# Kernel tuning notes

Hardware: AMD Instinct MI355X
Metric: run time of the kernel (lower is better)

The kernel has to match this reference:

```python
import jax, jax.numpy as jnp
import numpy as np

B, S, HID = 1, 4096, 2048
H, KV, D = 16, 8, 128
EPS = 1e-6
ROPE_THETA = 10000.0


def _rms_norm(x, w, eps=EPS):
    # x: [..., D], normalize over last dim in fp32 like Qwen3 RMSNorm
    xf = x.astype(jnp.float32)
    var = jnp.mean(xf * xf, axis=-1, keepdims=True)
    return (xf * jax.lax.rsqrt(var + eps)).astype(x.dtype) * w


def _rotate_half(x):
    x1, x2 = jnp.split(x, 2, axis=-1)
    return jnp.concatenate([-x2, x1], axis=-1)


def setup_inputs() -> dict:
    key = jax.random.key(0)
    ks = jax.random.split(key, 6)
    hidden_states = jax.random.normal(ks[0], (B, S, HID), dtype=jnp.float32)
    wq = jax.random.normal(ks[1], (H * D, HID), dtype=jnp.float32) * 0.02
    wk = jax.random.normal(ks[2], (KV * D, HID), dtype=jnp.float32) * 0.02
    wv = jax.random.normal(ks[3], (KV * D, HID), dtype=jnp.float32) * 0.02
    wo = jax.random.normal(ks[4], (HID, H * D), dtype=jnp.float32) * 0.02
    q_norm_w = jnp.ones((D,), dtype=jnp.float32)
    k_norm_w = jnp.ones((D,), dtype=jnp.float32)
    # real rotary tables: inv_freq over half dim, duplicated (HF convention)
    inv_freq = 1.0 / (ROPE_THETA ** (jnp.arange(0, D, 2, dtype=jnp.float32) / D))
    pos = jnp.arange(S, dtype=jnp.float32)
    freqs = pos[:, None] * inv_freq[None, :]          # [S, D/2]
    emb = jnp.concatenate([freqs, freqs], axis=-1)    # [S, D]
    cos = jnp.cos(emb)[None].astype(jnp.float32)      # [B, S, D]
    sin = jnp.sin(emb)[None].astype(jnp.float32)
    return {"hidden_states": hidden_states, "cos": cos, "sin": sin,
            "wq": wq, "wk": wk, "wv": wv, "wo": wo,
            "q_norm_w": q_norm_w, "k_norm_w": k_norm_w}


def reference(hidden_states, cos, sin, wq, wk, wv, wo, q_norm_w, k_norm_w):
    b, s, _ = hidden_states.shape
    scaling = D ** -0.5
    # QKV projections (no bias), reshape to heads, QK RMSNorm, then [b, h, s, d]
    q = _rms_norm(jnp.einsum('bsh,oh->bso', hidden_states, wq).reshape(b, s, H, D), q_norm_w)
    k = _rms_norm(jnp.einsum('bsh,oh->bso', hidden_states, wk).reshape(b, s, KV, D), k_norm_w)
    v = jnp.einsum('bsh,oh->bso', hidden_states, wv).reshape(b, s, KV, D)
    q = q.transpose(0, 2, 1, 3)  # [b, H, s, d]
    k = k.transpose(0, 2, 1, 3)  # [b, KV, s, d]
    v = v.transpose(0, 2, 1, 3)
    # RoPE (cos/sin broadcast over head dim)
    c = cos[:, None, :, :]
    sn = sin[:, None, :, :]
    q = q * c + _rotate_half(q) * sn
    k = k * c + _rotate_half(k) * sn
    # GQA: repeat KV heads to H
    groups = H // KV
    k = jnp.repeat(k, groups, axis=1)
    v = jnp.repeat(v, groups, axis=1)
    # eager causal attention, softmax in fp32
    scores = jnp.einsum('bhqd,bhkd->bhqk', q, k) * scaling
    causal = jnp.tril(jnp.ones((s, s), dtype=bool))
    scores = jnp.where(causal[None, None], scores, jnp.finfo(jnp.float32).min)
    attn = jax.nn.softmax(scores.astype(jnp.float32), axis=-1).astype(q.dtype)
    out = jnp.einsum('bhqk,bhkd->bhqd', attn, v)
    out = out.transpose(0, 2, 1, 3).reshape(b, s, H * D)
    return jnp.einsum('bso,ho->bsh', out, wo)
```

## Files before the change

kernel.cpp:

```cpp
#include <hip/hip_runtime.h>
#include <hip/hip_bf16.h>

typedef __hip_bfloat16 bf16;
typedef __attribute__((ext_vector_type(8))) short short8;
typedef __attribute__((ext_vector_type(4))) float f32x4;

#define S_LEN 4096
#define HID_DIM 2048

#define QSCALE ((float)(0.08838834764831845 * 1.4426950408889634))

__device__ __forceinline__ void gld_lds16(const void* g, void* l) {
  __builtin_amdgcn_global_load_lds(
      (const __attribute__((address_space(1))) void*)g,
      (__attribute__((address_space(3))) void*)l, 16, 0, 0);
}

__device__ __forceinline__ float fexp2(float x) {
  return __builtin_amdgcn_exp2f(x);
}

__device__ __forceinline__ unsigned cvtpk_bf16(float lo, float hi) {
  unsigned r;
  asm("v_cvt_pk_bf16_f32 %0, %1, %2" : "=v"(r) : "v"(lo), "v"(hi));
  return r;
}

__global__ __launch_bounds__(256) void k_cvt(const float* __restrict__ src,
                                             bf16* __restrict__ dst, int n) {
  long i = ((long)blockIdx.x * 256 + threadIdx.x) * 8;
  if (i >= n) return;
  float4 a = *reinterpret_cast<const float4*>(src + i);
  float4 b = *reinterpret_cast<const float4*>(src + i + 4);
  float v[8] = {a.x, a.y, a.z, a.w, b.x, b.y, b.z, b.w};
  short8 o;
#pragma unroll
  for (int j = 0; j < 8; ++j) {
    bf16 h = __float2bfloat16(v[j]);
    o[j] = *reinterpret_cast<short*>(&h);
  }
  *reinterpret_cast<short8*>(dst + i) = o;
}

template <typename OutT>
__global__ __launch_bounds__(512, 1) void k_gemm256(
    const bf16* __restrict__ A, const bf16* __restrict__ B,
    OutT* __restrict__ C, int M, int N, int K) {
  __shared__ bf16 Al[2][256 * 64];
  __shared__ bf16 Bl[2][256 * 64];
  const int tid = threadIdx.x;
  const int lane = tid & 63;
  const int wid = tid >> 6;
  const int wr = wid >> 2;
  const int wc = wid & 3;
  const long brow = (long)blockIdx.y * 256;
  const long bcol = (long)blockIdx.x * 256;
  const int NT = K >> 6;

  auto stage = [&](int kt, int buf) {
    const bf16* At = A + brow * K + kt * 64;
    const bf16* Bt = B + bcol * K + kt * 64;
#pragma unroll
    for (int i = 0; i < 4; ++i) {
      const int ch = tid + i * 512;
      const int row = ch >> 3;
      const int j = (ch & 7) ^ (row & 7);
      gld_lds16(At + (size_t)row * K + j * 8, &Al[buf][(wid * 64 + i * 512) * 8]);
    }
#pragma unroll
    for (int i = 0; i < 4; ++i) {
      const int ch = tid + i * 512;
      const int row = ch >> 3;
      const int j = (ch & 7) ^ (row & 7);
      gld_lds16(Bt + (size_t)row * K + j * 8, &Bl[buf][(wid * 64 + i * 512) * 8]);
    }
  };

  f32x4 acc0[4][4], acc1[4][4];
#pragma unroll
  for (int m = 0; m < 4; ++m)
#pragma unroll
    for (int n = 0; n < 4; ++n) {
      acc0[m][n] = (f32x4){0.f, 0.f, 0.f, 0.f};
      acc1[m][n] = (f32x4){0.f, 0.f, 0.f, 0.f};
    }

  const int l15 = lane & 15;
  const int cp0 = ((lane >> 4) ^ (lane & 7)) * 8;
  const int cp1 = ((4 + (lane >> 4)) ^ (lane & 7)) * 8;

  stage(0, 0);
  stage(1, 1);
  asm volatile("s_waitcnt vmcnt(8)" ::: "memory");
  __builtin_amdgcn_s_barrier();

  for (int kt = 0; kt < NT; ++kt) {
    const bf16* Ab = &Al[kt & 1][0];
    const bf16* Bb = &Bl[kt & 1][0];
    short8 bB[4][2], aA[4][2];
#pragma unroll
    for (int n = 0; n < 4; ++n) {
      const int rb = (wc * 64 + n * 16 + l15) * 64;
      bB[n][0] = *reinterpret_cast<const short8*>(&Bb[rb + cp0]);
      bB[n][1] = *reinterpret_cast<const short8*>(&Bb[rb + cp1]);
    }
#pragma unroll
    for (int m = 0; m < 4; ++m) {
      const int ra = (wr * 128 + m * 16 + l15) * 64;
      aA[m][0] = *reinterpret_cast<const short8*>(&Ab[ra + cp0]);
      aA[m][1] = *reinterpret_cast<const short8*>(&Ab[ra + cp1]);
    }
    __builtin_amdgcn_s_setprio(1);
#pragma unroll
    for (int m = 0; m < 4; ++m)
#pragma unroll
      for (int n = 0; n < 4; ++n) {
        acc0[m][n] = __builtin_amdgcn_mfma_f32_16x16x32_bf16(aA[m][0], bB[n][0],
                                                             acc0[m][n], 0, 0, 0);
        acc0[m][n] = __builtin_amdgcn_mfma_f32_16x16x32_bf16(aA[m][1], bB[n][1],
                                                             acc0[m][n], 0, 0, 0);
      }
    __builtin_amdgcn_s_setprio(0);
#pragma unroll
    for (int m = 0; m < 4; ++m) {
      const int ra = (wr * 128 + 64 + m * 16 + l15) * 64;
      aA[m][0] = *reinterpret_cast<const short8*>(&Ab[ra + cp0]);
      aA[m][1] = *reinterpret_cast<const short8*>(&Ab[ra + cp1]);
    }
    __builtin_amdgcn_s_setprio(1);
#pragma unroll
    for (int m = 0; m < 4; ++m)
#pragma unroll
      for (int n = 0; n < 4; ++n) {
        acc1[m][n] = __builtin_amdgcn_mfma_f32_16x16x32_bf16(aA[m][0], bB[n][0],
                                                             acc1[m][n], 0, 0, 0);
        acc1[m][n] = __builtin_amdgcn_mfma_f32_16x16x32_bf16(aA[m][1], bB[n][1],
                                                             acc1[m][n], 0, 0, 0);
      }
    __builtin_amdgcn_s_setprio(0);

    if (kt + 1 < NT) {
      __builtin_amdgcn_s_barrier();
      if (kt + 2 < NT) {
        stage(kt + 2, kt & 1);
        asm volatile("s_waitcnt vmcnt(8)" ::: "memory");
      } else {
        asm volatile("s_waitcnt vmcnt(0)" ::: "memory");
      }
      __builtin_amdgcn_s_barrier();
    }
  }

#pragma unroll
  for (int mh = 0; mh < 2; ++mh) {
#pragma unroll
    for (int m = 0; m < 4; ++m) {
      const long r0 = brow + wr * 128 + mh * 64 + m * 16 + (lane >> 4) * 4;
#pragma unroll
      for (int n = 0; n < 4; ++n) {
        const long c0 = bcol + wc * 64 + n * 16 + l15;
        const f32x4 v = mh ? acc1[m][n] : acc0[m][n];
#pragma unroll
        for (int r = 0; r < 4; ++r) {
          if constexpr (sizeof(OutT) == 2)
            C[(r0 + r) * N + c0] = __float2bfloat16(v[r]);
          else
            C[(r0 + r) * N + c0] = v[r];
        }
      }
    }
  }
}

__global__ __launch_bounds__(512, 1) void k_gemm_op(
    const bf16* __restrict__ A, const bf16* __restrict__ B,
    float* __restrict__ C, int M, int N, int K) {
  __shared__ bf16 Al[2][256 * 64];
  __shared__ bf16 Bl[2][128 * 64];
  const int tid = threadIdx.x;
  const int lane = tid & 63;
  const int wid = tid >> 6;
  const int wr = wid >> 1;
  const int wc = wid & 1;
  const long brow = (long)blockIdx.y * 256;
  const long bcol = (long)blockIdx.x * 128;
  const int NT = K >> 6;

  auto stage = [&](int kt, int buf) {
    const bf16* At = A + brow * K + kt * 64;
    const bf16* Bt = B + bcol * K + kt * 64;
#pragma unroll
    for (int i = 0; i < 4; ++i) {
      const int ch = tid + i * 512;
      const int row = ch >> 3;
      const int j = (ch & 7) ^ (row & 7);
      gld_lds16(At + (size_t)row * K + j * 8, &Al[buf][(wid * 64 + i * 512) * 8]);
    }
#pragma unroll
    for (int i = 0; i < 2; ++i) {
      const int ch = tid + i * 512;
      const int row = ch >> 3;
      const int j = (ch & 7) ^ (row & 7);
      gld_lds16(Bt + (size_t)row * K + j * 8, &Bl[buf][(wid * 64 + i * 512) * 8]);
    }
  };

  f32x4 acc[4][4];
#pragma unroll
  for (int m = 0; m < 4; ++m)
#pragma unroll
    for (int n = 0; n < 4; ++n) acc[m][n] = (f32x4){0.f, 0.f, 0.f, 0.f};

  const int l15 = lane & 15;
  const int cp0 = ((lane >> 4) ^ (lane & 7)) * 8;
  const int cp1 = ((4 + (lane >> 4)) ^ (lane & 7)) * 8;

  stage(0, 0);
  stage(1, 1);
  asm volatile("s_waitcnt vmcnt(6)" ::: "memory");
  __builtin_amdgcn_s_barrier();

  for (int kt = 0; kt < NT; ++kt) {
    const bf16* Ab = &Al[kt & 1][0];
    const bf16* Bb = &Bl[kt & 1][0];
    short8 bB[4][2], aA[4][2];
#pragma unroll
    for (int n = 0; n < 4; ++n) {
      const int rb = (wc * 64 + n * 16 + l15) * 64;
      bB[n][0] = *reinterpret_cast<const short8*>(&Bb[rb + cp0]);
      bB[n][1] = *reinterpret_cast<const short8*>(&Bb[rb + cp1]);
    }
#pragma unroll
    for (int m = 0; m < 4; ++m) {
      const int ra = (wr * 64 + m * 16 + l15) * 64;
      aA[m][0] = *reinterpret_cast<const short8*>(&Ab[ra + cp0]);
      aA[m][1] = *reinterpret_cast<const short8*>(&Ab[ra + cp1]);
    }
    __builtin_amdgcn_s_setprio(1);
#pragma unroll
    for (int m = 0; m < 4; ++m)
#pragma unroll
      for (int n = 0; n < 4; ++n) {
        acc[m][n] = __builtin_amdgcn_mfma_f32_16x16x32_bf16(aA[m][0], bB[n][0],
                                                            acc[m][n], 0, 0, 0);
        acc[m][n] = __builtin_amdgcn_mfma_f32_16x16x32_bf16(aA[m][1], bB[n][1],
                                                            acc[m][n], 0, 0, 0);
      }
    __builtin_amdgcn_s_setprio(0);

    if (kt + 1 < NT) {
      __builtin_amdgcn_s_barrier();
      if (kt + 2 < NT) {
        stage(kt + 2, kt & 1);
        asm volatile("s_waitcnt vmcnt(6)" ::: "memory");
      } else {
        asm volatile("s_waitcnt vmcnt(0)" ::: "memory");
      }
      __builtin_amdgcn_s_barrier();
    }
  }

#pragma unroll
  for (int m = 0; m < 4; ++m) {
    const long r0 = brow + wr * 64 + m * 16 + (lane >> 4) * 4;
#pragma unroll
    for (int n = 0; n < 4; ++n) {
      const long c0 = bcol + wc * 64 + n * 16 + l15;
#pragma unroll
      for (int r = 0; r < 4; ++r) C[(r0 + r) * N + c0] = acc[m][n][r];
    }
  }
}

__global__ __launch_bounds__(256) void k_normrope(
    const bf16* __restrict__ QKVb, const float* __restrict__ cosb,
    const float* __restrict__ sinb, const float* __restrict__ qw,
    const float* __restrict__ kw, bf16* __restrict__ Qb, bf16* __restrict__ Kb,
    bf16* __restrict__ Vb) {
  const int lane = threadIdx.x & 63;
  const int row = blockIdx.x * 4 + (threadIdx.x >> 6);
  const int s = row >> 5;
  const int idx = row & 31;
  const bf16* src = QKVb + (size_t)s * 4096 + idx * 128;
  float x0 = __bfloat162float(src[lane]);
  float x1 = __bfloat162float(src[lane + 64]);
  if (idx < 24) {
    float ss = x0 * x0 + x1 * x1;
#pragma unroll
    for (int off = 1; off < 64; off <<= 1) ss += __shfl_xor(ss, off);
    const float rn = rsqrtf(ss * (1.f / 128.f) + 1e-6f);
    const float* w = (idx < 16) ? qw : kw;
    x0 = x0 * rn * w[lane];
    x1 = x1 * rn * w[lane + 64];
    const float c0 = cosb[(size_t)s * 128 + lane];
    const float c1 = cosb[(size_t)s * 128 + lane + 64];
    const float s0 = sinb[(size_t)s * 128 + lane];
    const float s1 = sinb[(size_t)s * 128 + lane + 64];
    float o0 = x0 * c0 - x1 * s0;
    float o1 = x1 * c1 + x0 * s1;
    if (idx < 16) { o0 *= QSCALE; o1 *= QSCALE; }
    bf16* dst = (idx < 16) ? (Qb + ((size_t)idx * S_LEN + s) * 128)
                           : (Kb + ((size_t)(idx - 16) * S_LEN + s) * 128);
    dst[lane] = __float2bfloat16(o0);
    dst[lane + 64] = __float2bfloat16(o1);
  } else {
    bf16* dst = Vb + ((size_t)(idx - 24) * S_LEN + s) * 128;
    dst[lane] = __float2bfloat16(x0);
    dst[lane + 64] = __float2bfloat16(x1);
  }
}

__global__ __launch_bounds__(256) void k_vt(const bf16* __restrict__ Vb,
                                            bf16* __restrict__ Vt) {
  __shared__ bf16 Lds[64][136];
  const int tid = threadIdx.x;
  const int s0 = blockIdx.x * 64;
  const int kv = blockIdx.y;
#pragma unroll
  for (int pass = 0; pass < 4; ++pass) {
    const int c = tid + pass * 256;
    const int r = c >> 4;
    const int off = (c & 15) * 8;
    *reinterpret_cast<short8*>(&Lds[r][off]) =
        *reinterpret_cast<const short8*>(
            &Vb[((size_t)kv * S_LEN + s0 + r) * 128 + off]);
  }
  __syncthreads();
#pragma unroll
  for (int pass = 0; pass < 4; ++pass) {
    const int c = tid + pass * 256;
    const int d = c >> 3;
    const int so = (c & 7) * 8;
    short8 o;
#pragma unroll
    for (int j = 0; j < 8; ++j) {
      bf16 e = Lds[so + j][d];
      o[j] = *reinterpret_cast<short*>(&e);
    }
    *reinterpret_cast<short8*>(&Vt[((size_t)kv * 128 + d) * S_LEN + s0 + so]) = o;
  }
}

__global__ __launch_bounds__(256) void k_attn(const bf16* __restrict__ Qb,
                                              const bf16* __restrict__ Kb,
                                              const bf16* __restrict__ Vt_g,
                                              bf16* __restrict__ AO) {
  __shared__ bf16 Kl[2][64 * 128];
  __shared__ bf16 Vl[2][128 * 64];
  __shared__ bf16 Pl[4][16 * 64];
  const int tid = threadIdx.x;
  const int lane = tid & 63;
  const int wv = tid >> 6;
  const int h = blockIdx.y;
  const int kvh = h >> 1;
  const int c16 = lane & 15;
  const int hi = lane >> 4;
  const int kk = hi * 8;

  const bf16* Kbase = Kb + (size_t)kvh * S_LEN * 128;
  const bf16* Vbase = Vt_g + (size_t)kvh * 128 * S_LEN;

  auto stage = [&](int t, int buf) {
    const bf16* Kt = Kbase + (size_t)t * 64 * 128;
    const bf16* Vt = Vbase + t * 64;
#pragma unroll
    for (int p = 0; p < 4; ++p) {
      const int ch = tid + p * 256;
      const int row = ch >> 4, cp = ch & 15;
      const int c = (cp & 8) | ((cp & 7) ^ (row & 7));
      gld_lds16(Kt + row * 128 + c * 8, &Kl[buf][(wv * 64 + p * 256) * 8]);
    }
#pragma unroll
    for (int p = 0; p < 4; ++p) {
      const int ch = tid + p * 256;
      const int d = ch >> 3, cp = ch & 7;
      const int c = cp ^ (d & 7);
      gld_lds16(Vt + (size_t)d * S_LEN + c * 8, &Vl[buf][(wv * 64 + p * 256) * 8]);
    }
  };

  for (int half = 0; half < 2; ++half) {
    const int qt = half ? (63 - blockIdx.x) : blockIdx.x;
    const int qrow = qt * 64 + wv * 16;
    const int grow = qrow + c16;

    __syncthreads();
    stage(0, 0);

    short8 qf[4];
    {
      const bf16* qp = Qb + ((size_t)h * S_LEN + grow) * 128 + kk;
#pragma unroll
      for (int ks = 0; ks < 4; ++ks)
        qf[ks] = *reinterpret_cast<const short8*>(qp + ks * 32);
    }

    f32x4 oacc[8];
#pragma unroll
    for (int i = 0; i < 8; ++i) oacc[i] = (f32x4){0.f, 0.f, 0.f, 0.f};
    float m_run = -1e30f;
    float l_part = 0.f;

    auto tile = [&](int t, int buf, bool mask) {
      f32x4 sacc[4];
#pragma unroll
      for (int nt = 0; nt < 4; ++nt) sacc[nt] = (f32x4){0.f, 0.f, 0.f, 0.f};
#pragma unroll
      for (int ks = 0; ks < 4; ++ks) {
#pragma unroll
        for (int nt = 0; nt < 4; ++nt) {
          const int row = nt * 16 + c16;
          const int ck = ks * 4 + hi;
          const int ckp = (ck & 8) | ((ck & 7) ^ (row & 7));
          short8 kf =
              *reinterpret_cast<const short8*>(&Kl[buf][row * 128 + ckp * 8]);
          sacc[nt] = __builtin_amdgcn_mfma_f32_16x16x32_bf16(kf, qf[ks],
                                                             sacc[nt], 0, 0, 0);
        }
      }

      float tm = -1e30f;
#pragma unroll
      for (int nt = 0; nt < 4; ++nt)
#pragma unroll
        for (int r = 0; r < 4; ++r) {
          float sv = sacc[nt][r];
          if (mask && (t * 64 + nt * 16 + 4 * hi + r > grow)) sv = -1e30f;
          sacc[nt][r] = sv;
          tm = fmaxf(tm, sv);
        }
      tm = fmaxf(tm, __shfl_xor(tm, 16));
      tm = fmaxf(tm, __shfl_xor(tm, 32));
      if (__any(tm > m_run + 8.f)) {
        const float mn = fmaxf(m_run, tm);
        const float alpha = fexp2(m_run - mn);
        m_run = mn;
        l_part *= alpha;
#pragma unroll
        for (int dn = 0; dn < 8; ++dn) oacc[dn] *= alpha;
      }

#pragma unroll
      for (int nt = 0; nt < 4; ++nt) {
        const float p0 = fexp2(sacc[nt][0] - m_run);
        const float p1 = fexp2(sacc[nt][1] - m_run);
        const float p2 = fexp2(sacc[nt][2] - m_run);
        const float p3 = fexp2(sacc[nt][3] - m_run);
        l_part += (p0 + p1) + (p2 + p3);
        const unsigned w0 = cvtpk_bf16(p0, p1);
        const unsigned w1 = cvtpk_bf16(p2, p3);
        const int chunk = (2 * nt + (hi >> 1)) ^ (c16 & 7);
        const int base = c16 * 64 + chunk * 8 + 4 * (hi & 1);
        *reinterpret_cast<unsigned*>(&Pl[wv][base]) = w0;
        *reinterpret_cast<unsigned*>(&Pl[wv][base + 2]) = w1;
      }

#pragma unroll
      for (int ks = 0; ks < 2; ++ks) {
        const int pc = (ks * 4 + hi) ^ (c16 & 7);
        short8 pf =
            *reinterpret_cast<const short8*>(&Pl[wv][c16 * 64 + pc * 8]);
#pragma unroll
        for (int dn = 0; dn < 8; ++dn) {
          const int d = dn * 16 + c16;
          const int cvp = (ks * 4 + hi) ^ (d & 7);
          short8 vf =
              *reinterpret_cast<const short8*>(&Vl[buf][d * 64 + cvp * 8]);
          oacc[dn] =
              __builtin_amdgcn_mfma_f32_16x16x32_bf16(vf, pf, oacc[dn], 0, 0, 0);
        }
      }
    };

    __syncthreads();
    int cur = 0;
    for (int t = 0; t < qt; ++t) {
      stage(t + 1, cur ^ 1);
      tile(t, cur, false);
      __syncthreads();
      cur ^= 1;
    }
    tile(qt, cur, true);

    float lt = l_part;
    lt += __shfl_xor(lt, 16);
    lt += __shfl_xor(lt, 32);
    const float inv = 1.f / lt;
    bf16* dst = AO + (size_t)grow * HID_DIM + h * 128;
#pragma unroll
    for (int dn = 0; dn < 8; ++dn) {
#pragma unroll
      for (int w = 0; w < 2; ++w) {
        const unsigned pk = cvtpk_bf16(oacc[dn][2 * w] * inv,
                                       oacc[dn][2 * w + 1] * inv);
        *reinterpret_cast<unsigned*>(&dst[dn * 16 + 4 * hi + 2 * w]) = pk;
      }
    }
  }
}

extern "C" void kernel_launch(void* const* d_in, const int* in_sizes, int n_in,
                              void* d_out, int out_size, void* d_ws,
                              size_t ws_size, hipStream_t stream) {
  (void)in_sizes; (void)n_in; (void)out_size; (void)ws_size;
  const float* hs = (const float*)d_in[0];
  const float* cosb = (const float*)d_in[1];
  const float* sinb = (const float*)d_in[2];
  const float* wq = (const float*)d_in[3];
  const float* wk = (const float*)d_in[4];
  const float* wv = (const float*)d_in[5];
  const float* wo = (const float*)d_in[6];
  const float* qnw = (const float*)d_in[7];
  const float* knw = (const float*)d_in[8];
  float* out = (float*)d_out;
  char* ws = (char*)d_ws;

  bf16* Ah = (bf16*)(ws + 0);
  bf16* Wqkv = (bf16*)(ws + 16777216);
  bf16* Wo = (bf16*)(ws + 33554432);
  bf16* QKVb = (bf16*)(ws + 41943040);
  bf16* Qb = (bf16*)(ws + 75497472);
  bf16* Kb = (bf16*)(ws + 92274688);
  bf16* Vb = (bf16*)(ws + 100663296);
  bf16* AO = (bf16*)(ws + 109051904);
  bf16* Vt = (bf16*)(ws + 125829120);

  auto cvt = [&](const float* s, bf16* d, long n) {
    k_cvt<<<dim3((unsigned)((n / 8 + 255) / 256)), dim3(256), 0, stream>>>(
        s, d, (int)n);
  };
  cvt(hs, Ah, (long)S_LEN * HID_DIM);
  cvt(wq, Wqkv, (long)2048 * 2048);
  cvt(wk, Wqkv + (long)2048 * 2048, (long)1024 * 2048);
  cvt(wv, Wqkv + (long)3072 * 2048, (long)1024 * 2048);
  cvt(wo, Wo, (long)2048 * 2048);

  k_gemm256<bf16><<<dim3(16, 16), dim3(512), 0, stream>>>(Ah, Wqkv, QKVb, 4096,
                                                          4096, 2048);
  k_normrope<<<dim3(32768), dim3(256), 0, stream>>>(QKVb, cosb, sinb, qnw, knw,
                                                    Qb, Kb, Vb);
  k_vt<<<dim3(64, 8), dim3(256), 0, stream>>>(Vb, Vt);
  k_attn<<<dim3(32, 16), dim3(256), 0, stream>>>(Qb, Kb, Vt, AO);
  k_gemm_op<<<dim3(16, 16), dim3(512), 0, stream>>>(AO, Wo, out, 4096, 2048,
                                                    2048);
}
```

Measured before the change: 284.2 us.

## Split attention KV range across block pairs with 32x32 MFMA and merge pass

Attention now uses 32x32x16 bf16 MFMAs with 128-row query groups per block. The P matrix is kept in registers and rearranged with permlane32 swaps, so the LDS round trip for P is gone. Each causal query group's KV range is split between two blocks that write fp32 partial outputs plus max/sum, and a new merge kernel combines them into bf16. This aims to raise MFMA efficiency and balance causal work, at the cost of extra fp32 partial traffic and an additional launch.

After: 333.8 us. +17.5%, slower.

```diff
diff --git a/kernel.cpp b/kernel.cpp
--- a/kernel.cpp
+++ b/kernel.cpp
@@ -4,6 +4,8 @@
 typedef __hip_bfloat16 bf16;
 typedef __attribute__((ext_vector_type(8))) short short8;
 typedef __attribute__((ext_vector_type(4))) float f32x4;
+typedef __attribute__((ext_vector_type(16))) float f32x16;
+typedef __attribute__((ext_vector_type(4))) int int4v;
 
 #define S_LEN 4096
 #define HID_DIM 2048
@@ -24,6 +26,10 @@
   unsigned r;
   asm("v_cvt_pk_bf16_f32 %0, %1, %2" : "=v"(r) : "v"(lo), "v"(hi));
   return r;
+}
+
+__device__ __forceinline__ void half_swap(unsigned& x, unsigned& y) {
+  asm volatile("v_permlane32_swap_b32 %0, %1" : "+v"(x), "+v"(y));
 }
 
 __global__ __launch_bounds__(256) void k_cvt(const float* __restrict__ src,
@@ -341,21 +347,21 @@
   }
 }
 
-__global__ __launch_bounds__(256) void k_attn(const bf16* __restrict__ Qb,
-                                              const bf16* __restrict__ Kb,
-                                              const bf16* __restrict__ Vt_g,
-                                              bf16* __restrict__ AO) {
+__global__ __launch_bounds__(256) void k_attn_part(
+    const bf16* __restrict__ Qb, const bf16* __restrict__ Kb,
+    const bf16* __restrict__ Vt_g, float* __restrict__ Opart,
+    float* __restrict__ ML) {
   __shared__ bf16 Kl[2][64 * 128];
   __shared__ bf16 Vl[2][128 * 64];
-  __shared__ bf16 Pl[4][16 * 64];
   const int tid = threadIdx.x;
   const int lane = tid & 63;
   const int wv = tid >> 6;
   const int h = blockIdx.y;
   const int kvh = h >> 1;
-  const int c16 = lane & 15;
-  const int hi = lane >> 4;
-  const int kk = hi * 8;
+  const int pr = blockIdx.x >> 1;
+  const int part = blockIdx.x & 1;
+  const int q32 = lane & 31;
+  const int hh = lane >> 5;
 
   const bf16* Kbase = Kb + (size_t)kvh * S_LEN * 128;
   const bf16* Vbase = Vt_g + (size_t)kvh * 128 * S_LEN;
@@ -366,70 +372,81 @@
 #pragma unroll
     for (int p = 0; p < 4; ++p) {
       const int ch = tid + p * 256;
-      const int row = ch >> 4, cp = ch & 15;
-      const int c = (cp & 8) | ((cp & 7) ^ (row & 7));
-      gld_lds16(Kt + row * 128 + c * 8, &Kl[buf][(wv * 64 + p * 256) * 8]);
+      const int row = ch >> 4, cpos = ch & 15;
+      const int j = (cpos & 8) |
+                    ((((cpos & 7) - 2 * ((row >> 3) & 3)) & 7) ^ (row & 7));
+      gld_lds16(Kt + row * 128 + j * 8, &Kl[buf][(wv * 64 + p * 256) * 8]);
     }
 #pragma unroll
     for (int p = 0; p < 4; ++p) {
       const int ch = tid + p * 256;
-      const int d = ch >> 3, cp = ch & 7;
-      const int c = cp ^ (d & 7);
-      gld_lds16(Vt + (size_t)d * S_LEN + c * 8, &Vl[buf][(wv * 64 + p * 256) * 8]);
+      const int d = ch >> 3, cpos = ch & 7;
+      const int j = (((cpos - 2 * ((d >> 3) & 3)) & 7)) ^ (d & 7);
+      gld_lds16(Vt + (size_t)d * S_LEN + j * 8, &Vl[buf][(wv * 64 + p * 256) * 8]);
     }
   };
 
-  for (int half = 0; half < 2; ++half) {
-    const int qt = half ? (63 - blockIdx.x) : blockIdx.x;
-    const int qrow = qt * 64 + wv * 16;
-    const int grow = qrow + c16;
-
-    __syncthreads();
-    stage(0, 0);
-
-    short8 qf[4];
+  for (int hf = 0; hf < 2; ++hf) {
+    const int g = hf ? (31 - pr) : pr;
+    const int qrow = g * 128 + wv * 32;
+    const int grow = qrow + q32;
+    const int t0 = part ? (g + 1) : 0;
+    const int t1 = part ? (2 * g + 2) : (g + 1);
+    const int diag = 2 * g + (wv >> 1);
+
+    if (hf) __syncthreads();
+    stage(t0, 0);
+
+    short8 qf[8];
     {
-      const bf16* qp = Qb + ((size_t)h * S_LEN + grow) * 128 + kk;
-#pragma unroll
-      for (int ks = 0; ks < 4; ++ks)
-        qf[ks] = *reinterpret_cast<const short8*>(qp + ks * 32);
-    }
-
-    f32x4 oacc[8];
-#pragma unroll
-    for (int i = 0; i < 8; ++i) oacc[i] = (f32x4){0.f, 0.f, 0.f, 0.f};
+      const bf16* qp = Qb + ((size_t)h * S_LEN + grow) * 128 + hh * 8;
+#pragma unroll
+      for (int ks = 0; ks < 8; ++ks)
+        qf[ks] = *reinterpret_cast<const short8*>(qp + ks * 16);
+    }
+
+    f32x16 oacc[4];
+#pragma unroll
+    for (int i = 0; i < 4; ++i)
+#pragma unroll
+      for (int r = 0; r < 16; ++r) oacc[i][r] = 0.f;
     float m_run = -1e30f;
     float l_part = 0.f;
 
     auto tile = [&](int t, int buf, bool mask) {
-      f32x4 sacc[4];
-#pragma unroll
-      for (int nt = 0; nt < 4; ++nt) sacc[nt] = (f32x4){0.f, 0.f, 0.f, 0.f};
-#pragma unroll
-      for (int ks = 0; ks < 4; ++ks) {
-#pragma unroll
-        for (int nt = 0; nt < 4; ++nt) {
-          const int row = nt * 16 + c16;
-          const int ck = ks * 4 + hi;
-          const int ckp = (ck & 8) | ((ck & 7) ^ (row & 7));
+      f32x16 sacc[2];
+#pragma unroll
+      for (int nt = 0; nt < 2; ++nt)
+#pragma unroll
+        for (int r = 0; r < 16; ++r) sacc[nt][r] = 0.f;
+#pragma unroll
+      for (int ks = 0; ks < 8; ++ks) {
+#pragma unroll
+        for (int nt = 0; nt < 2; ++nt) {
+          const int row = nt * 32 + q32;
+          const int ck = 2 * ks + hh;
+          const int cpos = (ck & 8) |
+                           ((((ck & 7) ^ (row & 7)) + 2 * ((row >> 3) & 3)) & 7);
           short8 kf =
-              *reinterpret_cast<const short8*>(&Kl[buf][row * 128 + ckp * 8]);
-          sacc[nt] = __builtin_amdgcn_mfma_f32_16x16x32_bf16(kf, qf[ks],
+              *reinterpret_cast<const short8*>(&Kl[buf][row * 128 + cpos * 8]);
+          sacc[nt] = __builtin_amdgcn_mfma_f32_32x32x16_bf16(kf, qf[ks],
                                                              sacc[nt], 0, 0, 0);
         }
       }
 
       float tm = -1e30f;
 #pragma unroll
-      for (int nt = 0; nt < 4; ++nt)
-#pragma unroll
-        for (int r = 0; r < 4; ++r) {
+      for (int nt = 0; nt < 2; ++nt)
+#pragma unroll
+        for (int r = 0; r < 16; ++r) {
           float sv = sacc[nt][r];
-          if (mask && (t * 64 + nt * 16 + 4 * hi + r > grow)) sv = -1e30f;
+          if (mask) {
+            const int kv = t * 64 + nt * 32 + (r & 3) + 8 * (r >> 2) + 4 * hh;
+            if (kv > grow) sv = -1e30f;
+          }
           sacc[nt][r] = sv;
           tm = fmaxf(tm, sv);
         }
-      tm = fmaxf(tm, __shfl_xor(tm, 16));
       tm = fmaxf(tm, __shfl_xor(tm, 32));
       if (__any(tm > m_run + 8.f)) {
         const float mn = fmaxf(m_run, tm);
@@ -437,66 +454,106 @@
         m_run = mn;
         l_part *= alpha;
 #pragma unroll
-        for (int dn = 0; dn < 8; ++dn) oacc[dn] *= alpha;
-      }
-
-#pragma unroll
-      for (int nt = 0; nt < 4; ++nt) {
-        const float p0 = fexp2(sacc[nt][0] - m_run);
-        const float p1 = fexp2(sacc[nt][1] - m_run);
-        const float p2 = fexp2(sacc[nt][2] - m_run);
-        const float p3 = fexp2(sacc[nt][3] - m_run);
-        l_part += (p0 + p1) + (p2 + p3);
-        const unsigned w0 = cvtpk_bf16(p0, p1);
-        const unsigned w1 = cvtpk_bf16(p2, p3);
-        const int chunk = (2 * nt + (hi >> 1)) ^ (c16 & 7);
-        const int base = c16 * 64 + chunk * 8 + 4 * (hi & 1);
-        *reinterpret_cast<unsigned*>(&Pl[wv][base]) = w0;
-        *reinterpret_cast<unsigned*>(&Pl[wv][base + 2]) = w1;
-      }
-
-#pragma unroll
-      for (int ks = 0; ks < 2; ++ks) {
-        const int pc = (ks * 4 + hi) ^ (c16 & 7);
-        short8 pf =
-            *reinterpret_cast<const short8*>(&Pl[wv][c16 * 64 + pc * 8]);
-#pragma unroll
-        for (int dn = 0; dn < 8; ++dn) {
-          const int d = dn * 16 + c16;
-          const int cvp = (ks * 4 + hi) ^ (d & 7);
+        for (int dn = 0; dn < 4; ++dn)
+#pragma unroll
+          for (int r = 0; r < 16; ++r) oacc[dn][r] *= alpha;
+      }
+#pragma unroll
+      for (int nt = 0; nt < 2; ++nt)
+#pragma unroll
+        for (int r = 0; r < 16; ++r) {
+          const float p = fexp2(sacc[nt][r] - m_run);
+          sacc[nt][r] = p;
+          l_part += p;
+        }
+
+#pragma unroll
+      for (int ks = 0; ks < 4; ++ks) {
+        const int nt = ks >> 1;
+        const int b0 = 2 * (ks & 1);
+        unsigned a00 = cvtpk_bf16(sacc[nt][4 * b0 + 0], sacc[nt][4 * b0 + 1]);
+        unsigned a01 = cvtpk_bf16(sacc[nt][4 * b0 + 2], sacc[nt][4 * b0 + 3]);
+        unsigned a10 = cvtpk_bf16(sacc[nt][4 * b0 + 4], sacc[nt][4 * b0 + 5]);
+        unsigned a11 = cvtpk_bf16(sacc[nt][4 * b0 + 6], sacc[nt][4 * b0 + 7]);
+        unsigned x00 = a00, y00 = a00; half_swap(x00, y00);
+        unsigned x01 = a01, y01 = a01; half_swap(x01, y01);
+        unsigned x10 = a10, y10 = a10; half_swap(x10, y10);
+        unsigned x11 = a11, y11 = a11; half_swap(x11, y11);
+        int4v pw;
+        pw[0] = (int)(hh ? x10 : x00);
+        pw[1] = (int)(hh ? x11 : x01);
+        pw[2] = (int)(hh ? y10 : y00);
+        pw[3] = (int)(hh ? y11 : y01);
+        const short8 pf = __builtin_bit_cast(short8, pw);
+#pragma unroll
+        for (int dn = 0; dn < 4; ++dn) {
+          const int d = dn * 32 + q32;
+          const int cv = 2 * ks + hh;
+          const int cpos = (((cv ^ (d & 7)) + 2 * ((d >> 3) & 3)) & 7);
           short8 vf =
-              *reinterpret_cast<const short8*>(&Vl[buf][d * 64 + cvp * 8]);
-          oacc[dn] =
-              __builtin_amdgcn_mfma_f32_16x16x32_bf16(vf, pf, oacc[dn], 0, 0, 0);
+              *reinterpret_cast<const short8*>(&Vl[buf][d * 64 + cpos * 8]);
+          oacc[dn] = __builtin_amdgcn_mfma_f32_32x32x16_bf16(vf, pf, oacc[dn],
+                                                             0, 0, 0);
         }
       }
     };
 
     __syncthreads();
     int cur = 0;
-    for (int t = 0; t < qt; ++t) {
+    for (int t = t0; t < t1 - 1; ++t) {
       stage(t + 1, cur ^ 1);
-      tile(t, cur, false);
+      if (t <= diag) tile(t, cur, t == diag);
       __syncthreads();
       cur ^= 1;
     }
-    tile(qt, cur, true);
-
-    float lt = l_part;
-    lt += __shfl_xor(lt, 16);
-    lt += __shfl_xor(lt, 32);
-    const float inv = 1.f / lt;
-    bf16* dst = AO + (size_t)grow * HID_DIM + h * 128;
-#pragma unroll
-    for (int dn = 0; dn < 8; ++dn) {
-#pragma unroll
-      for (int w = 0; w < 2; ++w) {
-        const unsigned pk = cvtpk_bf16(oacc[dn][2 * w] * inv,
-                                       oacc[dn][2 * w + 1] * inv);
-        *reinterpret_cast<unsigned*>(&dst[dn * 16 + 4 * hi + 2 * w]) = pk;
-      }
-    }
-  }
+    if (t1 - 1 <= diag) tile(t1 - 1, cur, (t1 - 1) == diag);
+
+    float lt = l_part + __shfl_xor(l_part, 32);
+    const int job = (h * 32 + g) * 2 + part;
+    float* Op = Opart + (size_t)job * 128 * 128;
+    float* MLp = ML + (size_t)job * 256;
+    const int rq = wv * 32 + q32;
+#pragma unroll
+    for (int dn = 0; dn < 4; ++dn)
+#pragma unroll
+      for (int b = 0; b < 4; ++b) {
+        float4 v;
+        v.x = oacc[dn][4 * b + 0];
+        v.y = oacc[dn][4 * b + 1];
+        v.z = oacc[dn][4 * b + 2];
+        v.w = oacc[dn][4 * b + 3];
+        *reinterpret_cast<float4*>(&Op[rq * 128 + dn * 32 + 8 * b + 4 * hh]) = v;
+      }
+    if (lane < 32) {
+      MLp[rq] = m_run;
+      MLp[128 + rq] = lt;
+    }
+  }
+}
+
+__global__ __launch_bounds__(256) void k_merge(const float* __restrict__ Opart,
+                                               const float* __restrict__ ML,
+                                               bf16* __restrict__ AO) {
+  const int idx = blockIdx.x * 4 + (threadIdx.x >> 6);
+  const int lane = threadIdx.x & 63;
+  const int h = idx >> 12;
+  const int s = idx & 4095;
+  const int g = s >> 7, rowin = s & 127;
+  const int j0 = (h * 32 + g) * 2;
+  const float m0 = ML[(size_t)j0 * 256 + rowin];
+  const float l0 = ML[(size_t)j0 * 256 + 128 + rowin];
+  const float m1 = ML[(size_t)(j0 + 1) * 256 + rowin];
+  const float l1 = ML[(size_t)(j0 + 1) * 256 + 128 + rowin];
+  const float mm = fmaxf(m0, m1);
+  const float a0 = fexp2(m0 - mm), a1 = fexp2(m1 - mm);
+  const float inv = 1.f / (l0 * a0 + l1 * a1);
+  const float2 o0 = *reinterpret_cast<const float2*>(
+      &Opart[((size_t)j0 * 128 + rowin) * 128 + lane * 2]);
+  const float2 o1 = *reinterpret_cast<const float2*>(
+      &Opart[((size_t)(j0 + 1) * 128 + rowin) * 128 + lane * 2]);
+  bf16* dst = AO + (size_t)s * HID_DIM + h * 128 + lane * 2;
+  dst[0] = __float2bfloat16((o0.x * a0 + o1.x * a1) * inv);
+  dst[1] = __float2bfloat16((o0.y * a0 + o1.y * a1) * inv);
 }
 
 extern "C" void kernel_launch(void* const* d_in, const int* in_sizes, int n_in,
@@ -517,13 +574,15 @@
 
   bf16* Ah = (bf16*)(ws + 0);
   bf16* Wqkv = (bf16*)(ws + 16777216);
-  bf16* Wo = (bf16*)(ws + 33554432);
-  bf16* QKVb = (bf16*)(ws + 41943040);
-  bf16* Qb = (bf16*)(ws + 75497472);
-  bf16* Kb = (bf16*)(ws + 92274688);
-  bf16* Vb = (bf16*)(ws + 100663296);
+  bf16* QKVb = (bf16*)(ws + 33554432);
+  bf16* Qb = (bf16*)(ws + 67108864);
+  bf16* Kb = (bf16*)(ws + 83886080);
+  bf16* Vb = (bf16*)(ws + 92274688);
+  bf16* Vt = (bf16*)(ws + 100663296);
   bf16* AO = (bf16*)(ws + 109051904);
-  bf16* Vt = (bf16*)(ws + 125829120);
+  bf16* Wo = (bf16*)(ws + 125829120);
+  float* Opart = (float*)(ws + 0);
+  float* ML = (float*)(ws + 92274688);
 
   auto cvt = [&](const float* s, bf16* d, long n) {
     k_cvt<<<dim3((unsigned)((n / 8 + 255) / 256)), dim3(256), 0, stream>>>(
@@ -540,7 +599,8 @@
   k_normrope<<<dim3(32768), dim3(256), 0, stream>>>(QKVb, cosb, sinb, qnw, knw,
                                                     Qb, Kb, Vb);
   k_vt<<<dim3(64, 8), dim3(256), 0, stream>>>(Vb, Vt);
-  k_attn<<<dim3(32, 16), dim3(256), 0, stream>>>(Qb, Kb, Vt, AO);
+  k_attn_part<<<dim3(32, 16), dim3(256), 0, stream>>>(Qb, Kb, Vt, Opart, ML);
+  k_merge<<<dim3(16384), dim3(256), 0, stream>>>(Opart, ML, AO);
   k_gemm_op<<<dim3(16, 16), dim3(512), 0, stream>>>(AO, Wo, out, 4096, 2048,
                                                     2048);
 }
```
